# Kernel optimization log

Hardware: AMD Instinct MI355X
Metric: run time of the kernel (lower is better)

Reference implementation:

```python
import jax, jax.numpy as jnp
import numpy as np

B, N, OBS = 512, 64, 256
H1, H2 = 4, 4
D = 128            # embed/key dim (d_k_1 = d_k_2 = 128)
O1 = D // H1       # 32, per-head value dim stage 1
O2 = D // H2       # 32, per-head value dim stage 2
IN2 = O1 * H1      # 128, input dim to stage 2
FOUT = 16          # final_output_dim


def setup_inputs() -> dict:
    key = jax.random.key(0)
    ks = jax.random.split(key, 22)
    g = lambda k, shp: (jax.random.normal(k, shp, dtype=jnp.float32) * 0.05)
    inp = {
        "states": jax.random.normal(ks[0], (B, N, OBS), dtype=jnp.float32),
        # stage 1 per-head params, stacked over heads
        "E1_w": g(ks[1], (H1, D, OBS)), "E1_b": g(ks[2], (H1, D)),
        "K1_w": g(ks[3], (H1, D, D)),   "K1_b": g(ks[4], (H1, D)),
        "Q1_w": g(ks[5], (H1, D, D)),   "Q1_b": g(ks[6], (H1, D)),
        "V1_w": g(ks[7], (H1, O1, D)),  "V1_b": g(ks[8], (H1, O1)),
        # stage 2 per-head params
        "E2_w": g(ks[9], (H2, D, IN2)), "E2_b": g(ks[10], (H2, D)),
        "K2_w": g(ks[11], (H2, D, D)),  "K2_b": g(ks[12], (H2, D)),
        "Q2_w": g(ks[13], (H2, D, D)),  "Q2_b": g(ks[14], (H2, D)),
        "V2_w": g(ks[15], (H2, O2, D)), "V2_b": g(ks[16], (H2, O2)),
        # final MLP policy head
        "F1_w": g(ks[17], (64, O2 * H2)), "F1_b": g(ks[18], (64,)),
        "F2_w": g(ks[19], (FOUT, 64)),    "F2_b": g(ks[20], (FOUT,)),
    }
    return inp


def _attn_block(x, Ew, Eb, Kw, Kb, Qw, Qb, Vw, Vb, d_k):
    # x: [B,N,I]; all head loops batched via leading head axis h
    se = jax.nn.leaky_relu(jnp.einsum('bni,hdi->hbnd', x, Ew) + Eb[:, None, None, :])  # [h,B,N,D]
    k = jnp.einsum('hbnd,hed->hbne', se, Kw) + Kb[:, None, None, :]
    q = jnp.einsum('hbnd,hed->hbne', se, Qw) + Qb[:, None, None, :]
    w = jax.nn.softmax(jnp.einsum('hbne,hbme->hbnm', q, k) / jnp.sqrt(jnp.float32(d_k)), axis=-1)  # [h,B,N,N]
    v = jax.nn.leaky_relu(jnp.einsum('hbnd,hod->hbno', se, Vw) + Vb[:, None, None, :])  # [h,B,N,O]
    att = jnp.einsum('hbnm,hbmo->hbno', w, v)
    h, b, n, o = att.shape
    return jnp.transpose(att, (1, 2, 0, 3)).reshape(b, n, h * o), w


def reference(states, E1_w, E1_b, K1_w, K1_b, Q1_w, Q1_b, V1_w, V1_b,
              E2_w, E2_b, K2_w, K2_b, Q2_w, Q2_b, V2_w, V2_b,
              F1_w, F1_b, F2_w, F2_b):
    x1, w1 = _attn_block(states, E1_w, E1_b, K1_w, K1_b, Q1_w, Q1_b, V1_w, V1_b, D)
    x2, w2 = _attn_block(x1, E2_w, E2_b, K2_w, K2_b, Q2_w, Q2_b, V2_w, V2_b, D)
    h = jax.nn.leaky_relu(jnp.einsum('bnf,of->bno', x2, F1_w) + F1_b)
    policy = jax.nn.softmax(jnp.einsum('bno,po->bnp', h, F2_w) + F2_b, axis=-1)
    return policy, w1, w2
```

## Files before the change

### kernel.cpp

```cpp
#include <hip/hip_runtime.h>

typedef __attribute__((ext_vector_type(8))) short short8;
typedef __attribute__((ext_vector_type(4))) float f32x4;
typedef __attribute__((ext_vector_type(2))) unsigned uint2v;

#define MFMA(a, b, c) __builtin_amdgcn_mfma_f32_16x16x32_bf16((a), (b), (c), 0, 0, 0)

__device__ __forceinline__ short f2bf(float f) {
    union { float f; unsigned u; } v; v.f = f;
    unsigned r = v.u + 0x7fffu + ((v.u >> 16) & 1u);
    return (short)(r >> 16);
}
__device__ __forceinline__ float bf2f(short s) {
    union { unsigned u; float f; } v; v.u = ((unsigned)(unsigned short)s) << 16; return v.f;
}
__device__ __forceinline__ unsigned pkbf(float lo, float hi) {
    return (unsigned)(unsigned short)f2bf(lo) | ((unsigned)(unsigned short)f2bf(hi) << 16);
}
__device__ __forceinline__ float lrelu(float v) { return (v >= 0.f) ? v : 0.01f * v; }

__device__ __forceinline__ void load_lds16(const void* g, void* l) {
    __builtin_amdgcn_global_load_lds((const __attribute__((address_space(1))) void*)g,
                                     (__attribute__((address_space(3))) void*)l, 16, 0, 0);
}

struct ConvArgs { const float* src[7]; int end[7]; };

__global__ __launch_bounds__(256) void conv_and_gt_kernel(ConvArgs a,
                                                          short* __restrict__ dstw,
                                                          short* __restrict__ dstx,
                                                          const float* __restrict__ Q1w, const float* __restrict__ K1w,
                                                          const float* __restrict__ Q1b,
                                                          const float* __restrict__ Q2w, const float* __restrict__ K2w,
                                                          const float* __restrict__ Q2b,
                                                          short* __restrict__ gt, float* __restrict__ wvec) {
    if (blockIdx.x < 8425) {
        int i4 = blockIdx.x * 256 + threadIdx.x;
        int seg = 0;
#pragma unroll
        for (int s = 0; s < 6; s++) seg += (i4 >= a.end[s]) ? 1 : 0;
        int base = (seg == 0) ? 0 : a.end[seg - 1];
        float4 v = ((const float4*)a.src[seg])[i4 - base];
        uint2v o = { pkbf(v.x, v.y), pkbf(v.z, v.w) };
        short* dst = (seg == 6) ? (dstx + (size_t)(i4 - a.end[5]) * 4)
                                : (dstw + (size_t)i4 * 4);
        *(uint2v*)dst = o;
    } else {
        int bid = blockIdx.x - 8425;
        const int s  = bid >> 8;
        const int h  = (bid >> 6) & 3;
        const int fg = bid & 63;
        const float* Qw = (s ? Q2w : Q1w) + (size_t)h * 16384;
        const float* Kw = (s ? K2w : K1w) + (size_t)h * 16384;
        const float* qb = (s ? Q2b : Q1b) + h * 128;
        const int f = fg * 2 + (threadIdx.x >> 7);
        const int e = threadIdx.x & 127;
        float acc = 0.f, accw = 0.f;
#pragma unroll 8
        for (int c = 0; c < 128; c++) {
            float kv = Kw[c * 128 + f];
            acc  = fmaf(Qw[c * 128 + e], kv, acc);
            accw = fmaf(qb[c], kv, accw);
        }
        const float scale = 0.08838834764831845f;
        gt[((size_t)((s * 4 + h) * 128 + f)) * 128 + e] = f2bf(acc * scale);
        if (e == 0) wvec[(s * 4 + h) * 128 + f] = accw * scale;
    }
}

template<int IN>
__global__ __launch_bounds__(512, 4) void attn_stage_kernel(
    const short* __restrict__ xin,
    const short* __restrict__ Ew, const float* __restrict__ Eb,
    const short* __restrict__ Gt, const float* __restrict__ wvec,
    const short* __restrict__ Vw, const float* __restrict__ Vb,
    float* __restrict__ w_out,
    short* __restrict__ x_out)
{
    __shared__ short sm[38400];

    const int tid  = threadIdx.x;
    const int b    = blockIdx.x & 511;
    const int h0   = (blockIdx.x >> 9) << 1;
    const int wv8  = tid >> 6;
    const int hsel = wv8 >> 2;
    const int wvl  = wv8 & 3;
    const int h    = h0 + hsel;
    const int lane = tid & 63;
    const int quad = lane >> 4;
    const int l16  = lane & 15;
    const int myrow = wvl * 16 + l16;
    const int OFF_T  = hsel * 8192;
    const int OFF_SE = 16384 + hsel * 8704;
    const int OFF_VT = 33792 + hsel * 2304;
    constexpr int NK1 = IN / 32;

    {
        const short* xg = xin + (size_t)b * 64 * IN;
#pragma unroll
        for (int t = 0; t < IN / 64; t++) {
            int base  = wv8 * 8 * IN + t * 512;
            int off   = base + lane * 8;
            int row   = off / IN;
            int chunk = (off % IN) >> 3;
            int src   = row * IN + ((chunk ^ (row & 7)) << 3);
            load_lds16(xg + src, &sm[base]);
        }
    }

    short8 ebf[NK1 * 2];
    {
        const short* ewh = Ew + (size_t)h * 128 * IN;
#pragma unroll
        for (int k0i = 0; k0i < NK1; k0i++)
#pragma unroll
            for (int j = 0; j < 2; j++)
                ebf[k0i * 2 + j] = *(const short8*)(ewh + (size_t)(wvl * 32 + j * 16 + l16) * IN + k0i * 32 + quad * 8);
    }
    __syncthreads();

    short8 gtf[8];

    {
        f32x4 acc[4][2];
#pragma unroll
        for (int j = 0; j < 2; j++) {
            f32x4 eb4 = *(const f32x4*)&Eb[h * 128 + wvl * 32 + j * 16 + quad * 4];
#pragma unroll
            for (int i = 0; i < 4; i++) acc[i][j] = eb4;
        }
        __builtin_amdgcn_s_setprio(1);
#pragma unroll
        for (int k0i = 0; k0i < NK1; k0i++) {
            short8 x8[4];
#pragma unroll
            for (int i = 0; i < 4; i++) {
                int xrow = i * 16 + l16;
                int kc = k0i * 4 + quad;
                x8[i] = *(const short8*)&sm[xrow * IN + ((kc ^ (xrow & 7)) << 3)];
            }
#pragma unroll
            for (int i = 0; i < 4; i++)
#pragma unroll
                for (int j = 0; j < 2; j++)
                    acc[i][j] = MFMA(ebf[k0i * 2 + j], x8[i], acc[i][j]);
        }
        __builtin_amdgcn_s_setprio(0);
        {
            const short* gth = Gt + (size_t)h * 16384;
#pragma unroll
            for (int k0i = 0; k0i < 4; k0i++)
#pragma unroll
                for (int j = 0; j < 2; j++)
                    gtf[k0i * 2 + j] = *(const short8*)(gth + (size_t)(wvl * 32 + j * 16 + l16) * 128 + k0i * 32 + quad * 8);
        }
#pragma unroll
        for (int i = 0; i < 4; i++)
#pragma unroll
            for (int j = 0; j < 2; j++) {
                uint2v o = { pkbf(lrelu(acc[i][j][0]), lrelu(acc[i][j][1])),
                             pkbf(lrelu(acc[i][j][2]), lrelu(acc[i][j][3])) };
                *(uint2v*)&sm[OFF_SE + (i * 16 + l16) * 136 + wvl * 32 + j * 16 + quad * 4] = o;
            }
    }
    __syncthreads();

    {
        f32x4 tacc[4][2];
#pragma unroll
        for (int j = 0; j < 2; j++) {
            f32x4 wv4 = *(const f32x4*)&wvec[h * 128 + wvl * 32 + j * 16 + quad * 4];
#pragma unroll
            for (int i = 0; i < 4; i++) tacc[i][j] = wv4;
        }
        __builtin_amdgcn_s_setprio(1);
#pragma unroll
        for (int k0i = 0; k0i < 4; k0i++) {
            short8 se8[4];
#pragma unroll
            for (int i = 0; i < 4; i++)
                se8[i] = *(const short8*)&sm[OFF_SE + (i * 16 + l16) * 136 + k0i * 32 + quad * 8];
#pragma unroll
            for (int i = 0; i < 4; i++)
#pragma unroll
                for (int j = 0; j < 2; j++)
                    tacc[i][j] = MFMA(gtf[k0i * 2 + j], se8[i], tacc[i][j]);
        }
#pragma unroll
        for (int i = 0; i < 4; i++)
#pragma unroll
            for (int j = 0; j < 2; j++) {
                uint2v ot = { pkbf(tacc[i][j][0], tacc[i][j][1]),
                              pkbf(tacc[i][j][2], tacc[i][j][3]) };
                int trow = i * 16 + l16;
                int c = wvl * 4 + j * 2 + (quad >> 1);
                *(uint2v*)&sm[OFF_T + trow * 128 + ((c ^ (trow & 7)) << 3) + (quad & 1) * 4] = ot;
            }

        const short* vwh = Vw + (size_t)h * 32 * 128;
        const int n0v = (wvl >> 1) * 16, mrow = (wvl & 1) * 32;
        short8 vbf[4];
#pragma unroll
        for (int k0i = 0; k0i < 4; k0i++)
            vbf[k0i] = *(const short8*)(vwh + (size_t)(n0v + l16) * 128 + k0i * 32 + quad * 8);
        float vb = Vb[h * 32 + n0v + l16];
        f32x4 vacc[2];
        vacc[0] = (f32x4){vb, vb, vb, vb}; vacc[1] = vacc[0];
#pragma unroll
        for (int k0i = 0; k0i < 4; k0i++) {
            short8 a0 = *(const short8*)&sm[OFF_SE + (mrow + l16) * 136 + k0i * 32 + quad * 8];
            short8 a1 = *(const short8*)&sm[OFF_SE + (mrow + 16 + l16) * 136 + k0i * 32 + quad * 8];
            vacc[0] = MFMA(a0, vbf[k0i], vacc[0]);
            vacc[1] = MFMA(a1, vbf[k0i], vacc[1]);
        }
        __builtin_amdgcn_s_setprio(0);
#pragma unroll
        for (int i = 0; i < 2; i++) {
            uint2v ov = { pkbf(lrelu(vacc[i][0]), lrelu(vacc[i][1])),
                          pkbf(lrelu(vacc[i][2]), lrelu(vacc[i][3])) };
            *(uint2v*)&sm[OFF_VT + (n0v + l16) * 72 + mrow + i * 16 + quad * 4] = ov;
        }
    }
    __syncthreads();

    f32x4 lacc[4];
#pragma unroll
    for (int jj = 0; jj < 4; jj++) lacc[jj] = (f32x4){0.f, 0.f, 0.f, 0.f};
    __builtin_amdgcn_s_setprio(1);
#pragma unroll
    for (int k0 = 0; k0 < 128; k0 += 32) {
        int kc = (k0 >> 3) + quad;
        short8 tf = *(const short8*)&sm[OFF_T + myrow * 128 + ((kc ^ (myrow & 7)) << 3)];
#pragma unroll
        for (int jj = 0; jj < 4; jj++) {
            short8 af = *(const short8*)&sm[OFF_SE + (jj * 16 + l16) * 136 + k0 + quad * 8];
            lacc[jj] = MFMA(af, tf, lacc[jj]);
        }
    }
    __builtin_amdgcn_s_setprio(0);

    {
        float m01 = fmaxf(fmaxf(lacc[0][0], lacc[0][1]), fmaxf(lacc[0][2], lacc[0][3]));
        float m23 = fmaxf(fmaxf(lacc[1][0], lacc[1][1]), fmaxf(lacc[1][2], lacc[1][3]));
        float m45 = fmaxf(fmaxf(lacc[2][0], lacc[2][1]), fmaxf(lacc[2][2], lacc[2][3]));
        float m67 = fmaxf(fmaxf(lacc[3][0], lacc[3][1]), fmaxf(lacc[3][2], lacc[3][3]));
        float m = fmaxf(fmaxf(m01, m23), fmaxf(m45, m67));
        m = fmaxf(m, __shfl_xor(m, 16, 64));
        m = fmaxf(m, __shfl_xor(m, 32, 64));
        float sum = 0.f;
#pragma unroll
        for (int jj = 0; jj < 4; jj++)
#pragma unroll
            for (int r = 0; r < 4; r++) {
                float e = __expf(lacc[jj][r] - m);
                lacc[jj][r] = e; sum += e;
            }
        sum += __shfl_xor(sum, 16, 64);
        sum += __shfl_xor(sum, 32, 64);
        float inv = 1.0f / sum;
        float* wbase = w_out + ((size_t)(h * 512 + b)) * 4096 + (size_t)myrow * 64;
#pragma unroll
        for (int jj = 0; jj < 4; jj++) {
            f32x4 w4 = { lacc[jj][0] * inv, lacc[jj][1] * inv, lacc[jj][2] * inv, lacc[jj][3] * inv };
            uint2v o = { pkbf(w4[0], w4[1]), pkbf(w4[2], w4[3]) };
            int c = jj * 2 + (quad >> 1);
            *(uint2v*)&sm[OFF_T + myrow * 128 + ((c ^ (myrow & 7)) << 3) + (quad & 1) * 4] = o;
            __builtin_nontemporal_store(w4, (f32x4*)(wbase + jj * 16 + quad * 4));
        }
    }

    {
        f32x4 aacc[2]; aacc[0] = (f32x4){0.f, 0.f, 0.f, 0.f}; aacc[1] = aacc[0];
#pragma unroll
        for (int k0 = 0; k0 < 64; k0 += 32) {
            int kc = (k0 >> 3) + quad;
            short8 wf = *(const short8*)&sm[OFF_T + myrow * 128 + ((kc ^ (myrow & 7)) << 3)];
#pragma unroll
            for (int o = 0; o < 2; o++) {
                short8 vf = *(const short8*)&sm[OFF_VT + (o * 16 + l16) * 72 + k0 + quad * 8];
                aacc[o] = MFMA(vf, wf, aacc[o]);
            }
        }
        short* xob = x_out + (size_t)b * 8192 + (size_t)myrow * 128 + h * 32;
#pragma unroll
        for (int o = 0; o < 2; o++) {
            uint2v o8 = { pkbf(aacc[o][0], aacc[o][1]), pkbf(aacc[o][2], aacc[o][3]) };
            *(uint2v*)&xob[o * 16 + quad * 4] = o8;
        }
    }
}

#define H_LD 72
__global__ __launch_bounds__(256)
void final_mlp_mfma_kernel(const short* __restrict__ x2,
                           const short* __restrict__ F1wb,
                           const float* __restrict__ F1b,
                           const short* __restrict__ F2wb,
                           const float* __restrict__ F2b,
                           float* __restrict__ policy)
{
    __shared__ short hsm[4][16 * H_LD];
    const int tid  = threadIdx.x;
    const int wv   = tid >> 6;
    const int lane = tid & 63;
    const int quad = lane >> 4;
    const int l16  = lane & 15;
    const int rowbase = blockIdx.x * 64 + wv * 16;

    short8 a[4];
    const short* xrow = x2 + (size_t)(rowbase + l16) * 128;
#pragma unroll
    for (int k = 0; k < 4; k++) a[k] = *(const short8*)(xrow + k * 32 + quad * 8);
    f32x4 acc[4];
#pragma unroll
    for (int j = 0; j < 4; j++) acc[j] = *(const f32x4*)&F1b[j * 16 + quad * 4];
#pragma unroll
    for (int k = 0; k < 4; k++)
#pragma unroll
        for (int j = 0; j < 4; j++) {
            short8 b8 = *(const short8*)(F1wb + (size_t)(j * 16 + l16) * 128 + k * 32 + quad * 8);
            acc[j] = MFMA(b8, a[k], acc[j]);
        }
    short* hh = &hsm[wv][0];
#pragma unroll
    for (int j = 0; j < 4; j++) {
        uint2v o = { pkbf(lrelu(acc[j][0]), lrelu(acc[j][1])),
                     pkbf(lrelu(acc[j][2]), lrelu(acc[j][3])) };
        *(uint2v*)&hh[l16 * H_LD + j * 16 + quad * 4] = o;
    }
    __syncthreads();

    f32x4 lg = *(const f32x4*)&F2b[quad * 4];
#pragma unroll
    for (int k = 0; k < 2; k++) {
        short8 a2 = *(const short8*)(hh + l16 * H_LD + k * 32 + quad * 8);
        short8 b2 = *(const short8*)(F2wb + (size_t)l16 * 64 + k * 32 + quad * 8);
        lg = MFMA(b2, a2, lg);
    }
    float m = fmaxf(fmaxf(lg[0], lg[1]), fmaxf(lg[2], lg[3]));
    m = fmaxf(m, __shfl_xor(m, 16, 64));
    m = fmaxf(m, __shfl_xor(m, 32, 64));
    f32x4 e;
    float s = 0.f;
#pragma unroll
    for (int r = 0; r < 4; r++) { e[r] = __expf(lg[r] - m); s += e[r]; }
    s += __shfl_xor(s, 16, 64);
    s += __shfl_xor(s, 32, 64);
    float inv = 1.0f / s;
    f32x4 p4 = { e[0] * inv, e[1] * inv, e[2] * inv, e[3] * inv };
    __builtin_nontemporal_store(p4, (f32x4*)&policy[(size_t)(rowbase + l16) * 16 + quad * 4]);
}

extern "C" void kernel_launch(void* const* d_in, const int* in_sizes, int n_in,
                              void* d_out, int out_size, void* d_ws, size_t ws_size,
                              hipStream_t stream) {
    const float* states = (const float*)d_in[0];
    const float* E1w = (const float*)d_in[1];  const float* E1b = (const float*)d_in[2];
    const float* K1w = (const float*)d_in[3];  const float* K1b = (const float*)d_in[4];
    const float* Q1w = (const float*)d_in[5];  const float* Q1b = (const float*)d_in[6];
    const float* V1w = (const float*)d_in[7];  const float* V1b = (const float*)d_in[8];
    const float* E2w = (const float*)d_in[9];  const float* E2b = (const float*)d_in[10];
    const float* K2w = (const float*)d_in[11]; const float* K2b = (const float*)d_in[12];
    const float* Q2w = (const float*)d_in[13]; const float* Q2b = (const float*)d_in[14];
    const float* V2w = (const float*)d_in[15]; const float* V2b = (const float*)d_in[16];
    const float* F1w = (const float*)d_in[17]; const float* F1b = (const float*)d_in[18];
    const float* F2w = (const float*)d_in[19]; const float* F2b = (const float*)d_in[20];
    (void)K1b; (void)K2b;

    float* out    = (float*)d_out;
    float* policy = out;
    float* w1     = out + 512 * 64 * 16;
    float* w2     = w1 + 4 * 512 * 64 * 64;

    short* wsb = (short*)d_ws;
    short* x1b = wsb;
    short* xsb = wsb + 4194304;
    short* x2b = xsb;
    short* wts = wsb + 12582912;
    short* wE1 = wts;
    short* wV1 = wts + 131072;
    short* wE2 = wts + 147456;
    short* wV2 = wts + 212992;
    short* wF1 = wts + 229376;
    short* wF2 = wts + 237568;
    short* gt  = wts + 238592;
    float* wvec = (float*)(wts + 238592 + 131072);

    ConvArgs ca;
    ca.src[0] = E1w; ca.src[1] = V1w; ca.src[2] = E2w; ca.src[3] = V2w;
    ca.src[4] = F1w; ca.src[5] = F2w; ca.src[6] = states;
    ca.end[0] = 32768;  ca.end[1] = 36864;  ca.end[2] = 53248;  ca.end[3] = 57344;
    ca.end[4] = 59392;  ca.end[5] = 59648;  ca.end[6] = 2156800;
    conv_and_gt_kernel<<<8937, 256, 0, stream>>>(ca, wts, xsb,
                                                 Q1w, K1w, Q1b, Q2w, K2w, Q2b, gt, wvec);

    attn_stage_kernel<256><<<1024, 512, 0, stream>>>(
        xsb, wE1, E1b, gt, wvec, wV1, V1b, w1, x1b);
    attn_stage_kernel<128><<<1024, 512, 0, stream>>>(
        x1b, wE2, E2b, gt + 65536, wvec + 512, wV2, V2b, w2, x2b);
    final_mlp_mfma_kernel<<<512, 256, 0, stream>>>(x2b, wF1, F1b, wF2, F2b, policy);
}
```

Baseline: 217.9 us.

## Fuse states fp32-to-bf16 conversion into stage-1 attention load

Removes the separate conversion of the states tensor to bf16 in the prep kernel. The stage-1 attention kernel now reads fp32 states directly, converts them in registers and writes swizzled bf16 into LDS, which avoids a full bf16 round trip through global memory. It also folds log2(e) into the score scale so the softmax can use exp2f, and hoists the V-weight fragment loads earlier to overlap them with other work. The trade-off is that stage 1 loses its asynchronous LDS load path and reads twice as many bytes per element from global memory.

```diff
diff --git a/kernel.cpp b/kernel.cpp
--- a/kernel.cpp
+++ b/kernel.cpp
@@ -24,29 +24,26 @@
                                      (__attribute__((address_space(3))) void*)l, 16, 0, 0);
 }
 
-struct ConvArgs { const float* src[7]; int end[7]; };
+struct ConvArgs { const float* src[6]; int end[6]; };
 
 __global__ __launch_bounds__(256) void conv_and_gt_kernel(ConvArgs a,
                                                           short* __restrict__ dstw,
-                                                          short* __restrict__ dstx,
                                                           const float* __restrict__ Q1w, const float* __restrict__ K1w,
                                                           const float* __restrict__ Q1b,
                                                           const float* __restrict__ Q2w, const float* __restrict__ K2w,
                                                           const float* __restrict__ Q2b,
                                                           short* __restrict__ gt, float* __restrict__ wvec) {
-    if (blockIdx.x < 8425) {
+    if (blockIdx.x < 233) {
         int i4 = blockIdx.x * 256 + threadIdx.x;
         int seg = 0;
 #pragma unroll
-        for (int s = 0; s < 6; s++) seg += (i4 >= a.end[s]) ? 1 : 0;
+        for (int s = 0; s < 5; s++) seg += (i4 >= a.end[s]) ? 1 : 0;
         int base = (seg == 0) ? 0 : a.end[seg - 1];
         float4 v = ((const float4*)a.src[seg])[i4 - base];
         uint2v o = { pkbf(v.x, v.y), pkbf(v.z, v.w) };
-        short* dst = (seg == 6) ? (dstx + (size_t)(i4 - a.end[5]) * 4)
-                                : (dstw + (size_t)i4 * 4);
-        *(uint2v*)dst = o;
+        *(uint2v*)(dstw + (size_t)i4 * 4) = o;
     } else {
-        int bid = blockIdx.x - 8425;
+        int bid = blockIdx.x - 233;
         const int s  = bid >> 8;
         const int h  = (bid >> 6) & 3;
         const int fg = bid & 63;
@@ -62,15 +59,15 @@
             acc  = fmaf(Qw[c * 128 + e], kv, acc);
             accw = fmaf(qb[c], kv, accw);
         }
-        const float scale = 0.08838834764831845f;
+        const float scale = 0.12751743f;
         gt[((size_t)((s * 4 + h) * 128 + f)) * 128 + e] = f2bf(acc * scale);
         if (e == 0) wvec[(s * 4 + h) * 128 + f] = accw * scale;
     }
 }
 
-template<int IN>
+template<int IN, bool XF32>
 __global__ __launch_bounds__(512, 4) void attn_stage_kernel(
-    const short* __restrict__ xin,
+    const void* __restrict__ xin,
     const short* __restrict__ Ew, const float* __restrict__ Eb,
     const short* __restrict__ Gt, const float* __restrict__ wvec,
     const short* __restrict__ Vw, const float* __restrict__ Vb,
@@ -95,8 +92,23 @@
     const int OFF_VT = 33792 + hsel * 2304;
     constexpr int NK1 = IN / 32;
 
-    {
-        const short* xg = xin + (size_t)b * 64 * IN;
+    if constexpr (XF32) {
+        const float* xb = (const float*)xin + (size_t)b * 64 * IN;
+        constexpr int CPR = IN / 8;
+#pragma unroll
+        for (int it = 0; it < 64 * CPR / 512; it++) {
+            int idx = tid + 512 * it;
+            int row = idx / CPR, c = idx % CPR;
+            const float* src = xb + row * IN + c * 8;
+            float4 a0 = *(const float4*)src;
+            float4 a1 = *(const float4*)(src + 4);
+            union { unsigned u[4]; short8 s; } o;
+            o.u[0] = pkbf(a0.x, a0.y); o.u[1] = pkbf(a0.z, a0.w);
+            o.u[2] = pkbf(a1.x, a1.y); o.u[3] = pkbf(a1.z, a1.w);
+            *(short8*)&sm[row * IN + ((c ^ (row & 7)) << 3)] = o.s;
+        }
+    } else {
+        const short* xg = (const short*)xin + (size_t)b * 64 * IN;
 #pragma unroll
         for (int t = 0; t < IN / 64; t++) {
             int base  = wv8 * 8 * IN + t * 512;
@@ -120,6 +132,8 @@
     __syncthreads();
 
     short8 gtf[8];
+    short8 vbf[4];
+    const int n0v = (wvl >> 1) * 16, mrow = (wvl & 1) * 32;
 
     {
         f32x4 acc[4][2];
@@ -153,6 +167,10 @@
 #pragma unroll
                 for (int j = 0; j < 2; j++)
                     gtf[k0i * 2 + j] = *(const short8*)(gth + (size_t)(wvl * 32 + j * 16 + l16) * 128 + k0i * 32 + quad * 8);
+            const short* vwh = Vw + (size_t)h * 32 * 128;
+#pragma unroll
+            for (int k0i = 0; k0i < 4; k0i++)
+                vbf[k0i] = *(const short8*)(vwh + (size_t)(n0v + l16) * 128 + k0i * 32 + quad * 8);
         }
 #pragma unroll
         for (int i = 0; i < 4; i++)
@@ -197,12 +215,6 @@
                 *(uint2v*)&sm[OFF_T + trow * 128 + ((c ^ (trow & 7)) << 3) + (quad & 1) * 4] = ot;
             }
 
-        const short* vwh = Vw + (size_t)h * 32 * 128;
-        const int n0v = (wvl >> 1) * 16, mrow = (wvl & 1) * 32;
-        short8 vbf[4];
-#pragma unroll
-        for (int k0i = 0; k0i < 4; k0i++)
-            vbf[k0i] = *(const short8*)(vwh + (size_t)(n0v + l16) * 128 + k0i * 32 + quad * 8);
         float vb = Vb[h * 32 + n0v + l16];
         f32x4 vacc[2];
         vacc[0] = (f32x4){vb, vb, vb, vb}; vacc[1] = vacc[0];
@@ -252,7 +264,7 @@
         for (int jj = 0; jj < 4; jj++)
 #pragma unroll
             for (int r = 0; r < 4; r++) {
-                float e = __expf(lacc[jj][r] - m);
+                float e = exp2f(lacc[jj][r] - m);
                 lacc[jj][r] = e; sum += e;
             }
         sum += __shfl_xor(sum, 16, 64);
@@ -374,9 +386,8 @@
 
     short* wsb = (short*)d_ws;
     short* x1b = wsb;
-    short* xsb = wsb + 4194304;
-    short* x2b = xsb;
-    short* wts = wsb + 12582912;
+    short* x2b = wsb + 4194304;
+    short* wts = wsb + 8388608;
     short* wE1 = wts;
     short* wV1 = wts + 131072;
     short* wE2 = wts + 147456;
@@ -388,15 +399,15 @@
 
     ConvArgs ca;
     ca.src[0] = E1w; ca.src[1] = V1w; ca.src[2] = E2w; ca.src[3] = V2w;
-    ca.src[4] = F1w; ca.src[5] = F2w; ca.src[6] = states;
+    ca.src[4] = F1w; ca.src[5] = F2w;
     ca.end[0] = 32768;  ca.end[1] = 36864;  ca.end[2] = 53248;  ca.end[3] = 57344;
-    ca.end[4] = 59392;  ca.end[5] = 59648;  ca.end[6] = 2156800;
-    conv_and_gt_kernel<<<8937, 256, 0, stream>>>(ca, wts, xsb,
-                                                 Q1w, K1w, Q1b, Q2w, K2w, Q2b, gt, wvec);
-
-    attn_stage_kernel<256><<<1024, 512, 0, stream>>>(
-        xsb, wE1, E1b, gt, wvec, wV1, V1b, w1, x1b);
-    attn_stage_kernel<128><<<1024, 512, 0, stream>>>(
-        x1b, wE2, E2b, gt + 65536, wvec + 512, wV2, V2b, w2, x2b);
+    ca.end[4] = 59392;  ca.end[5] = 59648;
+    conv_and_gt_kernel<<<745, 256, 0, stream>>>(ca, wts,
+                                                Q1w, K1w, Q1b, Q2w, K2w, Q2b, gt, wvec);
+
+    attn_stage_kernel<256, true><<<1024, 512, 0, stream>>>(
+        (const void*)states, wE1, E1b, gt, wvec, wV1, V1b, w1, x1b);
+    attn_stage_kernel<128, false><<<1024, 512, 0, stream>>>(
+        (const void*)x1b, wE2, E2b, gt + 65536, wvec + 512, wV2, V2b, w2, x2b);
     final_mlp_mfma_kernel<<<512, 256, 0, stream>>>(x2b, wF1, F1b, wF2, F2b, policy);
 }
```

Measured after the change: 209.8 us. 1.04x faster.
